# Performance work log

Hardware: AMD Instinct MI355X
Metric: run time of the kernel (lower is better)

## Reference

```python
import jax, jax.numpy as jnp
import numpy as np

N = 50000   # nodes
E = 600000  # edges
D = 128     # emb_dim
L = 5       # num_layers
ATOM_DIMS = np.array([119, 4, 11, 13, 11, 7, 13, 2, 9]) + 5   # per-feature vocab (+5 as in source)
BOND_DIMS = np.array([7, 22, 2]) + 5
BL_CENTERS = np.arange(0.0, 2.0, 0.1, dtype=np.float32)   # 20 centers, gamma 10
PR_CENTERS = np.arange(0.0, 1.0, 0.05, dtype=np.float32)  # 20 centers, gamma 1
BL_GAMMA = 10.0
PR_GAMMA = 1.0
BN_EPS = 1e-5


def setup_inputs() -> dict:
    key = jax.random.key(0)
    ks = jax.random.split(key, 16)
    scale = 1.0 / np.sqrt(D)
    atom_off = jnp.asarray(np.concatenate([[0], np.cumsum(ATOM_DIMS)[:-1]]), jnp.int32)
    bond_off = jnp.asarray(np.concatenate([[0], np.cumsum(BOND_DIMS)[:-1]]), jnp.int32)
    return {
        "x": jax.random.randint(ks[0], (N, 9), 0, 7, dtype=jnp.int32),
        "edge_index": jax.random.randint(ks[1], (2, E), 0, N, dtype=jnp.int32),
        "edge_attr_int": jax.random.randint(ks[2], (E, 3), 0, 7, dtype=jnp.int32),
        "edge_attr_float": jax.random.uniform(ks[3], (E, 2), dtype=jnp.float32),
        "atom_off": atom_off,
        "bond_off": bond_off,
        "atom_emb": jax.random.normal(ks[4], (int(ATOM_DIMS.sum()), D), jnp.float32) * scale,
        "bond_emb": jax.random.normal(ks[5], (L, int(BOND_DIMS.sum()), D), jnp.float32) * scale,
        "W_bl": jax.random.normal(ks[6], (L, len(BL_CENTERS), D), jnp.float32) * scale,
        "b_bl": jnp.zeros((L, D), jnp.float32),
        "W_pr": jax.random.normal(ks[7], (L, len(PR_CENTERS), D), jnp.float32) * scale,
        "b_pr": jnp.zeros((L, D), jnp.float32),
        "mlp_W1": jax.random.normal(ks[8], (L, D, D), jnp.float32) * scale,
        "mlp_b1": jnp.zeros((L, D), jnp.float32),
        "bn1_g": jnp.ones((L, D), jnp.float32),
        "bn1_b": jnp.zeros((L, D), jnp.float32),
        "mlp_W2": jax.random.normal(ks[9], (L, D, D), jnp.float32) * scale,
        "mlp_b2": jnp.zeros((L, D), jnp.float32),
        "eps_gin": jnp.zeros((L,), jnp.float32),
        "bn_g": jnp.ones((L, D), jnp.float32),
        "bn_b": jnp.zeros((L, D), jnp.float32),
    }


def _bn(h, g, b):
    # BatchNorm1d, training-mode batch statistics over the node axis
    m = h.mean(0)
    v = h.var(0)
    return (h - m) * jax.lax.rsqrt(v + BN_EPS) * g + b


def _rbf(x, centers, gamma):
    # exp(-gamma * (x - c)^2): [E] -> [E, n_centers]
    return jnp.exp(-gamma * jnp.square(x[:, None] - centers[None, :]))


def reference(x, edge_index, edge_attr_int, edge_attr_float, atom_off, bond_off,
              atom_emb, bond_emb, W_bl, b_bl, W_pr, b_pr,
              mlp_W1, mlp_b1, bn1_g, bn1_b, mlp_W2, mlp_b2,
              eps_gin, bn_g, bn_b):
    # AtomEncoder: sum of 9 categorical embeddings (flat table + offsets)
    h = atom_emb[x + atom_off[None, :]].sum(1)  # [N, D]
    src, dst = edge_index[0], edge_index[1]
    bl = _rbf(edge_attr_float[:, 0], jnp.asarray(BL_CENTERS), BL_GAMMA)  # [E, 20]
    pr = _rbf(edge_attr_float[:, 1], jnp.asarray(PR_CENTERS), PR_GAMMA)  # [E, 20]
    for l in range(L):
        # per-layer edge embedding: BondEncoder + BondFloatRBF
        e = bond_emb[l][edge_attr_int + bond_off[None, :]].sum(1)
        e = e + bl @ W_bl[l] + b_bl[l] + pr @ W_pr[l] + b_pr[l]
        # GINConv (aggr='add'): mlp((1+eps)*x + sum_j relu(x_j + e_ij))
        msg = jax.nn.relu(h[src] + e)                       # [E, D]
        agg = jax.ops.segment_sum(msg, dst, num_segments=N)  # [N, D]
        z = (1.0 + eps_gin[l]) * h + agg
        z = z @ mlp_W1[l] + mlp_b1[l]
        z = jax.nn.relu(_bn(z, bn1_g[l], bn1_b[l]))
        z = z @ mlp_W2[l] + mlp_b2[l]
        # outer per-layer BatchNorm; ReLU except last layer (drop_ratio=0)
        z = _bn(z, bn_g[l], bn_b[l])
        if l < L - 1:
            z = jax.nn.relu(z)
        h = z
    return h  # JK='last'
```

## Files before the change

### kernel.cpp

```cpp
#include <hip/hip_runtime.h>
#include <hip/hip_bf16.h>

#define GN 50000
#define GE 600000
#define DD 128
#define TQ 4096
#define NBOND 2268
#define TROWS (2*(TQ+1) + NBOND)
#define SCB 49
#define NBANK 16
#define SSET (NBANK*256)
#define NB 782
#define LDK 136

typedef __attribute__((ext_vector_type(8))) short short8;
typedef __attribute__((ext_vector_type(4))) unsigned short ushort4v;
typedef __attribute__((ext_vector_type(4))) float floatx4;

__device__ __forceinline__ unsigned short f2b(float f) {
    __hip_bfloat16 h = __float2bfloat16(f);
    return __builtin_bit_cast(unsigned short, h);
}
__device__ __forceinline__ float b2f_lo(unsigned int u) { return __uint_as_float(u << 16); }
__device__ __forceinline__ float b2f_hi(unsigned int u) { return __uint_as_float(u & 0xffff0000u); }
__device__ __forceinline__ float bs2f(short s) {
    return __uint_as_float(((unsigned int)(unsigned short)s) << 16);
}

__global__ __launch_bounds__(256) void atom_kernel(
    const int* __restrict__ x, const int* __restrict__ atom_off,
    const float* __restrict__ atom_emb, unsigned short* __restrict__ h)
{
    int t = blockIdx.x * 256 + threadIdx.x;
    if (t >= GN * DD) return;
    int n = t >> 7, d = t & 127;
    float s = 0.f;
#pragma unroll
    for (int f = 0; f < 9; f++) {
        int idx = x[n * 9 + f] + atom_off[f];
        s += atom_emb[idx * DD + d];
    }
    h[t] = f2b(s);
}

__global__ __launch_bounds__(256) void hist_kernel(const int* __restrict__ ei, int* __restrict__ count)
{
    int e = blockIdx.x * 256 + threadIdx.x;
    if (e < GE) atomicAdd(&count[ei[GE + e]], 1);
}

__global__ __launch_bounds__(1024) void scan1_kernel(
    const int* __restrict__ count, int* __restrict__ row_start, int* __restrict__ blocksum)
{
    __shared__ int sh[1024];
    int t = threadIdx.x;
    int idx = blockIdx.x * 1024 + t;
    int v = (idx < GN) ? count[idx] : 0;
    sh[t] = v;
    __syncthreads();
    for (int off = 1; off < 1024; off <<= 1) {
        int u = (t >= off) ? sh[t - off] : 0;
        __syncthreads();
        sh[t] += u;
        __syncthreads();
    }
    if (idx <= GN) row_start[idx] = (t == 0) ? 0 : sh[t - 1];
    if (t == 1023) blocksum[blockIdx.x] = sh[1023];
}

__global__ __launch_bounds__(64) void scan2_kernel(
    const int* __restrict__ blocksum, int* __restrict__ blockoff)
{
    int t = threadIdx.x;
    int v = (t < SCB) ? blocksum[t] : 0;
#pragma unroll
    for (int off = 1; off < 64; off <<= 1) {
        int u = __shfl_up(v, off);
        if (t >= off) v += u;
    }
    int e = __shfl_up(v, 1);
    if (t == 0) e = 0;
    if (t < SCB) blockoff[t] = e;
}

__global__ __launch_bounds__(1024) void scan3_kernel(
    int* __restrict__ row_start, const int* __restrict__ blockoff)
{
    int idx = blockIdx.x * 1024 + threadIdx.x;
    if (idx <= GN) row_start[idx] += blockoff[blockIdx.x];
}

__global__ __launch_bounds__(256) void scatter_kernel(
    const int* __restrict__ ei, const int* __restrict__ eai, const float* __restrict__ eaf,
    const int* __restrict__ row_start, int* __restrict__ fill, int4* __restrict__ ep)
{
    int e = blockIdx.x * 256 + threadIdx.x;
    if (e < GE) {
        int d = ei[GE + e];
        int p = row_start[d] + atomicAdd(&fill[d], 1);
        int src = ei[e];
        float x1 = eaf[2 * e], x2 = eaf[2 * e + 1];
        int q1 = (int)(x1 * (float)TQ + 0.5f); q1 = min(max(q1, 0), TQ);
        int q2 = (int)(x2 * (float)TQ + 0.5f); q2 = min(max(q2, 0), TQ);
        int b0 = eai[3 * e], b1 = eai[3 * e + 1], b2 = eai[3 * e + 2];
        ep[p] = make_int4(src, q1 | (q2 << 16), (b0 * 27 + b1) * 7 + b2, 0);
    }
}

__global__ __launch_bounds__(128) void tables_kernel(
    const float* __restrict__ W_bl, const float* __restrict__ b_bl,
    const float* __restrict__ W_pr, const float* __restrict__ b_pr,
    const float* __restrict__ bond_emb, const int* __restrict__ bond_off,
    unsigned short* __restrict__ tbl_bl, unsigned short* __restrict__ tbl_pr,
    unsigned short* __restrict__ tbl_bond)
{
    int l = blockIdx.x / TROWS;
    int b = blockIdx.x % TROWS;
    int d = threadIdx.x;
    const float* W_bl_l = W_bl + (size_t)l * 20 * DD;
    const float* W_pr_l = W_pr + (size_t)l * 20 * DD;
    const float* bemb_l = bond_emb + (size_t)l * 46 * DD;
    if (b < (TQ + 1)) {
        float xq = b * (1.0f / TQ);
        float s = b_bl[(size_t)l * DD + d] + b_pr[(size_t)l * DD + d];
#pragma unroll
        for (int k = 0; k < 20; k++) {
            float dl = xq - 0.1f * k;
            s += __expf(-10.f * dl * dl) * W_bl_l[k * DD + d];
        }
        tbl_bl[((size_t)l * (TQ + 1) + b) * DD + d] = f2b(s);
    } else if (b < 2 * (TQ + 1)) {
        int q = b - (TQ + 1);
        float xq = q * (1.0f / TQ);
        float s = 0.f;
#pragma unroll
        for (int k = 0; k < 20; k++) {
            float dl = xq - 0.05f * k;
            s += __expf(-dl * dl) * W_pr_l[k * DD + d];
        }
        tbl_pr[((size_t)l * (TQ + 1) + q) * DD + d] = f2b(s);
    } else {
        int r = b - 2 * (TQ + 1);
        int b0 = r / 189;
        int rem = r % 189;
        int b1 = rem / 7, b2 = rem % 7;
        tbl_bond[((size_t)l * NBOND + r) * DD + d] =
            f2b(bemb_l[(b0 + bond_off[0]) * DD + d]
              + bemb_l[(b1 + bond_off[1]) * DD + d]
              + bemb_l[(b2 + bond_off[2]) * DD + d]);
    }
}

__global__ __launch_bounds__(256) void wfrag_kernel(
    const float* __restrict__ W1, const float* __restrict__ W2,
    unsigned short* __restrict__ wf_hi, unsigned short* __restrict__ wf_lo)
{
    int t = blockIdx.x * 256 + threadIdx.x;
    if (t >= 10 * 2048) return;
    int mat = t >> 11;
    int rem = t & 2047;
    int kt = rem >> 9;
    int rem2 = rem & 511;
    int nt = rem2 >> 6;
    int lane = rem2 & 63;
    const float* src = (mat & 1) ? (W2 + (size_t)(mat >> 1) * DD * DD)
                                 : (W1 + (size_t)(mat >> 1) * DD * DD);
    int n = nt * 16 + (lane & 15);
    int k0 = kt * 32 + (lane >> 4) * 8;
    size_t base = (size_t)mat * 16384 + (size_t)((kt * 8 + nt) * 64 + lane) * 8;
#pragma unroll
    for (int j = 0; j < 8; j++) {
        float w = src[(size_t)(k0 + j) * DD + n];
        unsigned short hi = f2b(w);
        wf_hi[base + j] = hi;
        wf_lo[base + j] = f2b(w - bs2f((short)hi));
    }
}

template <int BN>
__global__ __launch_bounds__(256) void edge_kernel(
    const int4* __restrict__ ep,
    const unsigned short* __restrict__ tbl_bl, const unsigned short* __restrict__ tbl_pr,
    const unsigned short* __restrict__ tbl_bond,
    const unsigned short* __restrict__ hsrc, const int* __restrict__ row_start,
    const float* __restrict__ eps_gin, int layer,
    const float* __restrict__ stats_prev, const float* __restrict__ g_prev,
    const float* __restrict__ b_prev,
    float* __restrict__ A)
{
    __shared__ float sc_s[DD], tr_s[DD];
    int tid = threadIdx.x;
    if (BN) {
        if (tid < DD) {
            float s = 0.f, q = 0.f;
#pragma unroll
            for (int bk = 0; bk < NBANK; bk++) {
                s += stats_prev[bk * 256 + tid];
                q += stats_prev[bk * 256 + 128 + tid];
            }
            float m = s * (1.0f / GN);
            float v = q * (1.0f / GN) - m * m;
            float sc = g_prev[tid] * rsqrtf(v + 1e-5f);
            sc_s[tid] = sc;
            tr_s[tid] = b_prev[tid] - m * sc;
        }
        __syncthreads();
    }

    int wid = __builtin_amdgcn_readfirstlane(tid >> 6);
    int lane = tid & 63;
    float sc0 = 1.f, tr0 = 0.f, sc1 = 1.f, tr1 = 0.f;
    if (BN) {
        sc0 = sc_s[2 * lane];     tr0 = tr_s[2 * lane];
        sc1 = sc_s[2 * lane + 1]; tr1 = tr_s[2 * lane + 1];
    }

    int n = blockIdx.x * 4 + wid;
    int s0 = __builtin_amdgcn_readfirstlane(row_start[n]);
    int s1 = __builtin_amdgcn_readfirstlane(row_start[n + 1]);
    const unsigned int* hu = (const unsigned int*)hsrc;
    const unsigned int* tb = (const unsigned int*)tbl_bl;
    const unsigned int* tp = (const unsigned int*)tbl_pr;
    const unsigned int* tg = (const unsigned int*)tbl_bond;
    float a0 = 0.f, a1 = 0.f;

    auto meta = [&](int pb, int4 (&mm)[4]) {
#pragma unroll
        for (int j = 0; j < 4; j++) mm[j] = ep[pb + j];
    };
    auto issue = [&](const int4 (&mm)[4], unsigned int (&ub)[4], unsigned int (&up)[4],
                     unsigned int (&ug)[4], unsigned int (&uh)[4]) {
#pragma unroll
        for (int j = 0; j < 4; j++) {
            ub[j] = tb[(size_t)(mm[j].y & 0xffff) * 64 + lane];
            up[j] = tp[(size_t)((unsigned)mm[j].y >> 16) * 64 + lane];
            ug[j] = tg[(size_t)mm[j].z * 64 + lane];
            uh[j] = hu[(size_t)mm[j].x * 64 + lane];
        }
    };
    auto consume = [&](const unsigned int (&ub)[4], const unsigned int (&up)[4],
                       const unsigned int (&ug)[4], const unsigned int (&uh)[4]) {
#pragma unroll
        for (int j = 0; j < 4; j++) {
            float h0, h1;
            if (BN) {
                h0 = fmaxf(fmaf(b2f_lo(uh[j]), sc0, tr0), 0.f);
                h1 = fmaxf(fmaf(b2f_hi(uh[j]), sc1, tr1), 0.f);
            } else {
                h0 = b2f_lo(uh[j]);
                h1 = b2f_hi(uh[j]);
            }
            a0 += fmaxf(h0 + b2f_lo(ub[j]) + b2f_lo(up[j]) + b2f_lo(ug[j]), 0.f);
            a1 += fmaxf(h1 + b2f_hi(ub[j]) + b2f_hi(up[j]) + b2f_hi(ug[j]), 0.f);
        }
    };

    int cnt = s1 - s0;
    int nfull = cnt >> 2;
    {
        int4 mA[4], mB[4];
        unsigned int ubA[4], upA[4], ugA[4], uhA[4];
        unsigned int ubB[4], upB[4], ugB[4], uhB[4];
        if (nfull > 0) {
            meta(s0, mA);
            issue(mA, ubA, upA, ugA, uhA);
            int i = 1;
            for (; i + 1 < nfull; i += 2) {
                meta(s0 + i * 4, mB);
                meta(s0 + (i + 1) * 4, mA);
                issue(mB, ubB, upB, ugB, uhB);
                consume(ubA, upA, ugA, uhA);
                issue(mA, ubA, upA, ugA, uhA);
                consume(ubB, upB, ugB, uhB);
            }
            if (i < nfull) {
                meta(s0 + i * 4, mB);
                issue(mB, ubB, upB, ugB, uhB);
                consume(ubA, upA, ugA, uhA);
                consume(ubB, upB, ugB, uhB);
            } else {
                consume(ubA, upA, ugA, uhA);
            }
        }
    }
    for (int p = s0 + nfull * 4; p < s1; p++) {
        int4 m0 = ep[p];
        unsigned int ub0 = tb[(size_t)(m0.y & 0xffff) * 64 + lane];
        unsigned int up0 = tp[(size_t)((unsigned)m0.y >> 16) * 64 + lane];
        unsigned int ug0 = tg[(size_t)m0.z * 64 + lane];
        unsigned int uh0 = hu[(size_t)m0.x * 64 + lane];
        float h00, h01;
        if (BN) {
            h00 = fmaxf(fmaf(b2f_lo(uh0), sc0, tr0), 0.f);
            h01 = fmaxf(fmaf(b2f_hi(uh0), sc1, tr1), 0.f);
        } else {
            h00 = b2f_lo(uh0);
            h01 = b2f_hi(uh0);
        }
        a0 += fmaxf(h00 + b2f_lo(ub0) + b2f_lo(up0) + b2f_lo(ug0), 0.f);
        a1 += fmaxf(h01 + b2f_hi(ub0) + b2f_hi(up0) + b2f_hi(ug0), 0.f);
    }

    float eps1 = 1.f + eps_gin[layer];
    unsigned int un = hu[(size_t)n * 64 + lane];
    float n0, n1;
    if (BN) {
        n0 = fmaxf(fmaf(b2f_lo(un), sc0, tr0), 0.f);
        n1 = fmaxf(fmaf(b2f_hi(un), sc1, tr1), 0.f);
    } else {
        n0 = b2f_lo(un);
        n1 = b2f_hi(un);
    }
    a0 += eps1 * n0;
    a1 += eps1 * n1;
    float2 o; o.x = a0; o.y = a1;
    *(float2*)(A + (size_t)n * DD + 2 * lane) = o;
}

template <int MODE>
__global__ __launch_bounds__(256) void gemm_kernel(
    const float* __restrict__ Asrc,
    const unsigned short* __restrict__ wf_hi, const unsigned short* __restrict__ wf_lo,
    const float* __restrict__ bias,
    unsigned short* __restrict__ Cbf, float* __restrict__ Cf32, int out_bf16,
    const float* __restrict__ stats_in, const float* __restrict__ bn_g,
    const float* __restrict__ bn_b, float* __restrict__ stats_out)
{
    __shared__ unsigned short Ahi[64 * LDK];
    __shared__ unsigned short Alo[64 * LDK];
    __shared__ float sc_s[DD], tr_s[DD];
    int tid = threadIdx.x, wid = tid >> 6, lane = tid & 63;
    int row0 = blockIdx.x * 64;

    if (MODE == 1) {
        if (tid < DD) {
            float s = 0.f, q = 0.f;
#pragma unroll
            for (int bk = 0; bk < NBANK; bk++) {
                s += stats_in[bk * 256 + tid];
                q += stats_in[bk * 256 + 128 + tid];
            }
            float m = s * (1.0f / GN);
            float v = q * (1.0f / GN) - m * m;
            float sc = bn_g[tid] * rsqrtf(v + 1e-5f);
            sc_s[tid] = sc;
            tr_s[tid] = bn_b[tid] - m * sc;
        }
        __syncthreads();
    }

    {
        const float* g = Asrc + (size_t)row0 * DD;
#pragma unroll
        for (int i = 0; i < 8; i++) {
            int idx = i * 1024 + tid * 4;
            float4 v = *(const float4*)(g + idx);
            int r = idx >> 7, c = idx & 127;
            if (MODE == 1) {
                v.x = fmaxf(v.x * sc_s[c]     + tr_s[c],     0.f);
                v.y = fmaxf(v.y * sc_s[c + 1] + tr_s[c + 1], 0.f);
                v.z = fmaxf(v.z * sc_s[c + 2] + tr_s[c + 2], 0.f);
                v.w = fmaxf(v.w * sc_s[c + 3] + tr_s[c + 3], 0.f);
            }
            ushort4v hi, lo;
            hi[0] = f2b(v.x); lo[0] = f2b(v.x - bs2f((short)hi[0]));
            hi[1] = f2b(v.y); lo[1] = f2b(v.y - bs2f((short)hi[1]));
            hi[2] = f2b(v.z); lo[2] = f2b(v.z - bs2f((short)hi[2]));
            hi[3] = f2b(v.w); lo[3] = f2b(v.w - bs2f((short)hi[3]));
            *(ushort4v*)(Ahi + r * LDK + c) = hi;
            *(ushort4v*)(Alo + r * LDK + c) = lo;
        }
    }
    __syncthreads();

    int quad = lane >> 4, l16 = lane & 15;
    floatx4 acc[4][2];
#pragma unroll
    for (int rt = 0; rt < 4; rt++)
#pragma unroll
        for (int nt = 0; nt < 2; nt++) acc[rt][nt] = (floatx4){0.f, 0.f, 0.f, 0.f};

    const short8* bhp = (const short8*)wf_hi;
    const short8* blp = (const short8*)wf_lo;
#pragma unroll
    for (int kt = 0; kt < 4; kt++) {
        short8 ahi[4], alo[4];
        int kb = kt * 32 + quad * 8;
#pragma unroll
        for (int rt = 0; rt < 4; rt++) {
            int ro = (rt * 16 + l16) * LDK + kb;
            ahi[rt] = *(const short8*)(Ahi + ro);
            alo[rt] = *(const short8*)(Alo + ro);
        }
#pragma unroll
        for (int nt = 0; nt < 2; nt++) {
            int ntg = wid * 2 + nt;
            short8 bhi = bhp[(kt * 8 + ntg) * 64 + lane];
            short8 blo = blp[(kt * 8 + ntg) * 64 + lane];
#pragma unroll
            for (int rt = 0; rt < 4; rt++) {
                acc[rt][nt] = __builtin_amdgcn_mfma_f32_16x16x32_bf16(ahi[rt], bhi, acc[rt][nt], 0, 0, 0);
                acc[rt][nt] = __builtin_amdgcn_mfma_f32_16x16x32_bf16(alo[rt], bhi, acc[rt][nt], 0, 0, 0);
                acc[rt][nt] = __builtin_amdgcn_mfma_f32_16x16x32_bf16(ahi[rt], blo, acc[rt][nt], 0, 0, 0);
            }
        }
    }

    int bank = blockIdx.x & (NBANK - 1);
#pragma unroll
    for (int nt = 0; nt < 2; nt++) {
        int col = (wid * 2 + nt) * 16 + l16;
        float bv = bias[col];
        float s = 0.f, q = 0.f;
#pragma unroll
        for (int rt = 0; rt < 4; rt++) {
#pragma unroll
            for (int v = 0; v < 4; v++) {
                int r = row0 + rt * 16 + quad * 4 + v;
                float o = acc[rt][nt][v] + bv;
                if (r < GN) {
                    s += o; q += o * o;
                    if (MODE == 1 && out_bf16) Cbf[(size_t)r * DD + col] = f2b(o);
                    else                       Cf32[(size_t)r * DD + col] = o;
                }
            }
        }
        s += __shfl_xor(s, 16); s += __shfl_xor(s, 32);
        q += __shfl_xor(q, 16); q += __shfl_xor(q, 32);
        if (lane < 16) {
            atomicAdd(&stats_out[bank * 256 + col], s);
            atomicAdd(&stats_out[bank * 256 + 128 + col], q);
        }
    }
}

__global__ __launch_bounds__(256) void bn_apply_kernel(
    const float* __restrict__ Z, const float* __restrict__ stats2,
    const float* __restrict__ g, const float* __restrict__ b,
    float* __restrict__ fout)
{
    __shared__ float sc_s[DD], tr_s[DD];
    int tid = threadIdx.x;
    if (tid < DD) {
        float s = 0.f, q = 0.f;
#pragma unroll
        for (int bk = 0; bk < NBANK; bk++) {
            s += stats2[bk * 256 + tid];
            q += stats2[bk * 256 + 128 + tid];
        }
        float m = s * (1.0f / GN);
        float v = q * (1.0f / GN) - m * m;
        float sc = g[tid] * rsqrtf(v + 1e-5f);
        sc_s[tid] = sc;
        tr_s[tid] = b[tid] - m * sc;
    }
    __syncthreads();
    const int total = GN * DD;
    for (int t = blockIdx.x * 256 + tid; t < total; t += gridDim.x * 256) {
        int c = t & 127;
        fout[t] = Z[t] * sc_s[c] + tr_s[c];
    }
}

extern "C" void kernel_launch(void* const* d_in, const int* in_sizes, int n_in,
                              void* d_out, int out_size, void* d_ws, size_t ws_size,
                              hipStream_t stream)
{
    const int*   x        = (const int*)d_in[0];
    const int*   ei       = (const int*)d_in[1];
    const int*   eai      = (const int*)d_in[2];
    const float* eaf      = (const float*)d_in[3];
    const int*   atom_off = (const int*)d_in[4];
    const int*   bond_off = (const int*)d_in[5];
    const float* atom_emb = (const float*)d_in[6];
    const float* bond_emb = (const float*)d_in[7];
    const float* W_bl     = (const float*)d_in[8];
    const float* b_bl     = (const float*)d_in[9];
    const float* W_pr     = (const float*)d_in[10];
    const float* b_pr     = (const float*)d_in[11];
    const float* W1       = (const float*)d_in[12];
    const float* b1       = (const float*)d_in[13];
    const float* bn1g     = (const float*)d_in[14];
    const float* bn1b     = (const float*)d_in[15];
    const float* W2       = (const float*)d_in[16];
    const float* b2       = (const float*)d_in[17];
    const float* eps_gin  = (const float*)d_in[18];
    const float* bng      = (const float*)d_in[19];
    const float* bnb      = (const float*)d_in[20];
    float* out = (float*)d_out;

    char* p = (char*)d_ws;
    unsigned short* h_bf  = (unsigned short*)p;  p += (size_t)GN * DD * 2;
    unsigned short* z2_bf = (unsigned short*)p;  p += (size_t)GN * DD * 2;
    float* A              = (float*)p;           p += (size_t)GN * DD * 4;
    float* z1             = (float*)p;           p += (size_t)GN * DD * 4;
    float* z2f            = (float*)p;           p += (size_t)GN * DD * 4;
    unsigned short* tbl_bl   = (unsigned short*)p;  p += (size_t)5 * (TQ + 1) * DD * 2;
    unsigned short* tbl_pr   = (unsigned short*)p;  p += (size_t)5 * (TQ + 1) * DD * 2;
    unsigned short* tbl_bond = (unsigned short*)p;  p += (size_t)5 * NBOND * DD * 2;
    unsigned short* wf_hi    = (unsigned short*)p;  p += (size_t)10 * 16384 * 2;
    unsigned short* wf_lo    = (unsigned short*)p;  p += (size_t)10 * 16384 * 2;
    float* stats_all = (float*)p;  p += (size_t)10 * SSET * 4;
    int* count    = (int*)p;    p += (size_t)GN * 4;
    int* fill     = (int*)p;    p += (size_t)GN * 4;
    int* row_start= (int*)p;    p += (size_t)(GN + 1) * 4;
    int* blocksum = (int*)p;    p += (size_t)SCB * 4;
    int* blockoff = (int*)p;    p += (size_t)SCB * 4;
    p = (char*)(((size_t)p + 15) & ~(size_t)15);
    int4* ep      = (int4*)p;   p += (size_t)GE * 16;

    hipMemsetAsync(count, 0, (size_t)GN * 4, stream);
    hipMemsetAsync(fill,  0, (size_t)GN * 4, stream);
    hipMemsetAsync(stats_all, 0, (size_t)10 * SSET * 4, stream);

    hist_kernel<<<(GE + 255) / 256, 256, 0, stream>>>(ei, count);
    scan1_kernel<<<SCB, 1024, 0, stream>>>(count, row_start, blocksum);
    scan2_kernel<<<1, 64, 0, stream>>>(blocksum, blockoff);
    scan3_kernel<<<SCB, 1024, 0, stream>>>(row_start, blockoff);
    scatter_kernel<<<(GE + 255) / 256, 256, 0, stream>>>(ei, eai, eaf, row_start, fill, ep);
    atom_kernel<<<(GN * DD + 255) / 256, 256, 0, stream>>>(x, atom_off, atom_emb, h_bf);
    wfrag_kernel<<<80, 256, 0, stream>>>(W1, W2, wf_hi, wf_lo);
    tables_kernel<<<5 * TROWS, 128, 0, stream>>>(
        W_bl, b_bl, W_pr, b_pr, bond_emb, bond_off, tbl_bl, tbl_pr, tbl_bond);

    for (int l = 0; l < 5; l++) {
        float* stats1 = stats_all + (size_t)(2 * l + 0) * SSET;
        float* stats2 = stats_all + (size_t)(2 * l + 1) * SSET;
        float* stats2_prev = stats_all + (size_t)(2 * (l - 1) + 1) * SSET;

        if (l == 0) {
            edge_kernel<0><<<GN / 4, 256, 0, stream>>>(
                ep, tbl_bl, tbl_pr, tbl_bond,
                h_bf, row_start, eps_gin, l,
                stats_all, bng, bnb, A);
        } else {
            edge_kernel<1><<<GN / 4, 256, 0, stream>>>(
                ep,
                tbl_bl + (size_t)l * (TQ + 1) * DD,
                tbl_pr + (size_t)l * (TQ + 1) * DD,
                tbl_bond + (size_t)l * NBOND * DD,
                z2_bf, row_start, eps_gin, l,
                stats2_prev,
                bng + (size_t)(l - 1) * DD,
                bnb + (size_t)(l - 1) * DD,
                A);
        }

        gemm_kernel<0><<<NB, 256, 0, stream>>>(
            A, wf_hi + (size_t)(l * 2 + 0) * 16384, wf_lo + (size_t)(l * 2 + 0) * 16384,
            b1 + (size_t)l * DD, nullptr, z1, 0,
            nullptr, nullptr, nullptr, stats1);

        gemm_kernel<1><<<NB, 256, 0, stream>>>(
            z1, wf_hi + (size_t)(l * 2 + 1) * 16384, wf_lo + (size_t)(l * 2 + 1) * 16384,
            b2 + (size_t)l * DD, z2_bf, z2f, (l < 4) ? 1 : 0,
            stats1, bn1g + (size_t)l * DD, bn1b + (size_t)l * DD, stats2);
    }

    bn_apply_kernel<<<1024, 256, 0, stream>>>(
        z2f, stats_all + (size_t)9 * SSET, bng + (size_t)4 * DD, bnb + (size_t)4 * DD, out);
}
```

Baseline: 668.7 us.

## Fuse edge aggregation and both MLP GEMMs into one cooperative per-layer kernel

Each layer's edge gather-aggregate, first GEMM with BN statistics, BN1+ReLU and second GEMM now run in a single cooperative kernel. Grid-wide syncs separate the phases, and the first GEMM's output stays in registers and LDS instead of a global z1 buffer. The last layer also applies the final BatchNorm in-kernel, which drops the separate bn_apply launch. This removes per-layer launches and the z1 global round trip, but the edge phase now runs as a grid-stride loop over only 782 blocks, so fewer waves are available to hide gather latency. The fallback path keeps the old kernels, with a simplified, unpipelined edge loop.

```diff
diff --git a/kernel.cpp b/kernel.cpp
--- a/kernel.cpp
+++ b/kernel.cpp
@@ -1,5 +1,8 @@
 #include <hip/hip_runtime.h>
 #include <hip/hip_bf16.h>
+#include <hip/hip_cooperative_groups.h>
+
+namespace cg = cooperative_groups;
 
 #define GN 50000
 #define GE 600000
@@ -177,6 +180,364 @@
     }
 }
 
+template <int L0, int LAST>
+__global__ __launch_bounds__(256, 4) void layer_kernel(
+    const int4* __restrict__ ep,
+    const unsigned short* __restrict__ tbl_bl, const unsigned short* __restrict__ tbl_pr,
+    const unsigned short* __restrict__ tbl_bond,
+    const unsigned short* __restrict__ hsrc, const int* __restrict__ row_start,
+    const float* __restrict__ eps_gin, int layer,
+    const float* __restrict__ stats_prev, const float* __restrict__ g_prev,
+    const float* __restrict__ b_prev,
+    float* __restrict__ A,
+    const unsigned short* __restrict__ wf1_hi, const unsigned short* __restrict__ wf1_lo,
+    const unsigned short* __restrict__ wf2_hi, const unsigned short* __restrict__ wf2_lo,
+    const float* __restrict__ bias1, const float* __restrict__ bias2,
+    float* __restrict__ stats1, float* __restrict__ stats2,
+    const float* __restrict__ bn1_g, const float* __restrict__ bn1_b,
+    const float* __restrict__ bn2_g, const float* __restrict__ bn2_b,
+    unsigned short* __restrict__ z2bf, float* __restrict__ out)
+{
+    __shared__ unsigned short Ahi[64 * LDK];
+    __shared__ unsigned short Alo[64 * LDK];
+    __shared__ float sc_s[DD], tr_s[DD];
+    cg::grid_group grid = cg::this_grid();
+    int tid = threadIdx.x, wid = tid >> 6, lane = tid & 63;
+
+    if (!L0) {
+        if (tid < DD) {
+            float s = 0.f, q = 0.f;
+#pragma unroll
+            for (int bk = 0; bk < NBANK; bk++) {
+                s += stats_prev[bk * 256 + tid];
+                q += stats_prev[bk * 256 + 128 + tid];
+            }
+            float m = s * (1.0f / GN);
+            float v = q * (1.0f / GN) - m * m;
+            float sc = g_prev[tid] * rsqrtf(v + 1e-5f);
+            sc_s[tid] = sc;
+            tr_s[tid] = b_prev[tid] - m * sc;
+        }
+        __syncthreads();
+    }
+    float sc0 = 1.f, tr0 = 0.f, sc1 = 1.f, tr1 = 0.f;
+    if (!L0) {
+        sc0 = sc_s[2 * lane];     tr0 = tr_s[2 * lane];
+        sc1 = sc_s[2 * lane + 1]; tr1 = tr_s[2 * lane + 1];
+    }
+
+    {
+        const unsigned int* hu = (const unsigned int*)hsrc;
+        const unsigned int* tb = (const unsigned int*)tbl_bl;
+        const unsigned int* tp = (const unsigned int*)tbl_pr;
+        const unsigned int* tg = (const unsigned int*)tbl_bond;
+        float eps1 = 1.f + eps_gin[layer];
+        int gw = blockIdx.x * 4 + wid;
+
+        for (int n = gw; n < GN; n += NB * 4) {
+            int s0 = __builtin_amdgcn_readfirstlane(row_start[n]);
+            int s1 = __builtin_amdgcn_readfirstlane(row_start[n + 1]);
+            float a0 = 0.f, a1 = 0.f;
+
+            auto meta = [&](int pb, int4 (&mm)[4]) {
+#pragma unroll
+                for (int j = 0; j < 4; j++) mm[j] = ep[pb + j];
+            };
+            auto issue = [&](const int4 (&mm)[4], unsigned int (&ub)[4], unsigned int (&up)[4],
+                             unsigned int (&ug)[4], unsigned int (&uh)[4]) {
+#pragma unroll
+                for (int j = 0; j < 4; j++) {
+                    ub[j] = tb[(size_t)(mm[j].y & 0xffff) * 64 + lane];
+                    up[j] = tp[(size_t)((unsigned)mm[j].y >> 16) * 64 + lane];
+                    ug[j] = tg[(size_t)mm[j].z * 64 + lane];
+                    uh[j] = hu[(size_t)mm[j].x * 64 + lane];
+                }
+            };
+            auto consume = [&](const unsigned int (&ub)[4], const unsigned int (&up)[4],
+                               const unsigned int (&ug)[4], const unsigned int (&uh)[4]) {
+#pragma unroll
+                for (int j = 0; j < 4; j++) {
+                    float h0, h1;
+                    if (!L0) {
+                        h0 = fmaxf(fmaf(b2f_lo(uh[j]), sc0, tr0), 0.f);
+                        h1 = fmaxf(fmaf(b2f_hi(uh[j]), sc1, tr1), 0.f);
+                    } else {
+                        h0 = b2f_lo(uh[j]);
+                        h1 = b2f_hi(uh[j]);
+                    }
+                    a0 += fmaxf(h0 + b2f_lo(ub[j]) + b2f_lo(up[j]) + b2f_lo(ug[j]), 0.f);
+                    a1 += fmaxf(h1 + b2f_hi(ub[j]) + b2f_hi(up[j]) + b2f_hi(ug[j]), 0.f);
+                }
+            };
+
+            int nfull = (s1 - s0) >> 2;
+            {
+                int4 mA[4], mB[4];
+                unsigned int ubA[4], upA[4], ugA[4], uhA[4];
+                unsigned int ubB[4], upB[4], ugB[4], uhB[4];
+                if (nfull > 0) {
+                    meta(s0, mA);
+                    issue(mA, ubA, upA, ugA, uhA);
+                    int i = 1;
+                    for (; i + 1 < nfull; i += 2) {
+                        meta(s0 + i * 4, mB);
+                        meta(s0 + (i + 1) * 4, mA);
+                        issue(mB, ubB, upB, ugB, uhB);
+                        consume(ubA, upA, ugA, uhA);
+                        issue(mA, ubA, upA, ugA, uhA);
+                        consume(ubB, upB, ugB, uhB);
+                    }
+                    if (i < nfull) {
+                        meta(s0 + i * 4, mB);
+                        issue(mB, ubB, upB, ugB, uhB);
+                        consume(ubA, upA, ugA, uhA);
+                        consume(ubB, upB, ugB, uhB);
+                    } else {
+                        consume(ubA, upA, ugA, uhA);
+                    }
+                }
+            }
+            for (int p = s0 + nfull * 4; p < s1; p++) {
+                int4 m0 = ep[p];
+                unsigned int ub0 = tb[(size_t)(m0.y & 0xffff) * 64 + lane];
+                unsigned int up0 = tp[(size_t)((unsigned)m0.y >> 16) * 64 + lane];
+                unsigned int ug0 = tg[(size_t)m0.z * 64 + lane];
+                unsigned int uh0 = hu[(size_t)m0.x * 64 + lane];
+                float h00, h01;
+                if (!L0) {
+                    h00 = fmaxf(fmaf(b2f_lo(uh0), sc0, tr0), 0.f);
+                    h01 = fmaxf(fmaf(b2f_hi(uh0), sc1, tr1), 0.f);
+                } else {
+                    h00 = b2f_lo(uh0);
+                    h01 = b2f_hi(uh0);
+                }
+                a0 += fmaxf(h00 + b2f_lo(ub0) + b2f_lo(up0) + b2f_lo(ug0), 0.f);
+                a1 += fmaxf(h01 + b2f_hi(ub0) + b2f_hi(up0) + b2f_hi(ug0), 0.f);
+            }
+
+            unsigned int un = hu[(size_t)n * 64 + lane];
+            float n0, n1;
+            if (!L0) {
+                n0 = fmaxf(fmaf(b2f_lo(un), sc0, tr0), 0.f);
+                n1 = fmaxf(fmaf(b2f_hi(un), sc1, tr1), 0.f);
+            } else {
+                n0 = b2f_lo(un);
+                n1 = b2f_hi(un);
+            }
+            a0 += eps1 * n0;
+            a1 += eps1 * n1;
+            float2 o; o.x = a0; o.y = a1;
+            *(float2*)(A + (size_t)n * DD + 2 * lane) = o;
+        }
+    }
+    __threadfence();
+    grid.sync();
+
+    int row0 = blockIdx.x * 64;
+    {
+        const float* g = A + (size_t)row0 * DD;
+#pragma unroll
+        for (int i = 0; i < 8; i++) {
+            int idx = i * 1024 + tid * 4;
+            float4 v = *(const float4*)(g + idx);
+            int r = idx >> 7, c = idx & 127;
+            ushort4v hi, lo;
+            hi[0] = f2b(v.x); lo[0] = f2b(v.x - bs2f((short)hi[0]));
+            hi[1] = f2b(v.y); lo[1] = f2b(v.y - bs2f((short)hi[1]));
+            hi[2] = f2b(v.z); lo[2] = f2b(v.z - bs2f((short)hi[2]));
+            hi[3] = f2b(v.w); lo[3] = f2b(v.w - bs2f((short)hi[3]));
+            *(ushort4v*)(Ahi + r * LDK + c) = hi;
+            *(ushort4v*)(Alo + r * LDK + c) = lo;
+        }
+    }
+    __syncthreads();
+
+    int quad = lane >> 4, l16 = lane & 15;
+    int bank = blockIdx.x & (NBANK - 1);
+    floatx4 acc1[4][2];
+#pragma unroll
+    for (int rt = 0; rt < 4; rt++)
+#pragma unroll
+        for (int nt = 0; nt < 2; nt++) acc1[rt][nt] = (floatx4){0.f, 0.f, 0.f, 0.f};
+    {
+        const short8* bhp = (const short8*)wf1_hi;
+        const short8* blp = (const short8*)wf1_lo;
+#pragma unroll
+        for (int kt = 0; kt < 4; kt++) {
+            short8 ahi[4], alo[4];
+            int kb = kt * 32 + quad * 8;
+#pragma unroll
+            for (int rt = 0; rt < 4; rt++) {
+                int ro = (rt * 16 + l16) * LDK + kb;
+                ahi[rt] = *(const short8*)(Ahi + ro);
+                alo[rt] = *(const short8*)(Alo + ro);
+            }
+#pragma unroll
+            for (int nt = 0; nt < 2; nt++) {
+                int ntg = wid * 2 + nt;
+                short8 bhi = bhp[(kt * 8 + ntg) * 64 + lane];
+                short8 blo = blp[(kt * 8 + ntg) * 64 + lane];
+#pragma unroll
+                for (int rt = 0; rt < 4; rt++) {
+                    acc1[rt][nt] = __builtin_amdgcn_mfma_f32_16x16x32_bf16(ahi[rt], bhi, acc1[rt][nt], 0, 0, 0);
+                    acc1[rt][nt] = __builtin_amdgcn_mfma_f32_16x16x32_bf16(alo[rt], bhi, acc1[rt][nt], 0, 0, 0);
+                    acc1[rt][nt] = __builtin_amdgcn_mfma_f32_16x16x32_bf16(ahi[rt], blo, acc1[rt][nt], 0, 0, 0);
+                }
+            }
+        }
+    }
+#pragma unroll
+    for (int nt = 0; nt < 2; nt++) {
+        int col = (wid * 2 + nt) * 16 + l16;
+        float bv = bias1[col];
+        float s = 0.f, q = 0.f;
+#pragma unroll
+        for (int rt = 0; rt < 4; rt++) {
+#pragma unroll
+            for (int v = 0; v < 4; v++) {
+                int r = row0 + rt * 16 + quad * 4 + v;
+                float o = acc1[rt][nt][v] + bv;
+                if (r < GN) { s += o; q += o * o; }
+            }
+        }
+        s += __shfl_xor(s, 16); s += __shfl_xor(s, 32);
+        q += __shfl_xor(q, 16); q += __shfl_xor(q, 32);
+        if (lane < 16) {
+            atomicAdd(&stats1[bank * 256 + col], s);
+            atomicAdd(&stats1[bank * 256 + 128 + col], q);
+        }
+    }
+    __threadfence();
+    grid.sync();
+
+    if (tid < DD) {
+        float s = 0.f, q = 0.f;
+#pragma unroll
+        for (int bk = 0; bk < NBANK; bk++) {
+            s += stats1[bk * 256 + tid];
+            q += stats1[bk * 256 + 128 + tid];
+        }
+        float m = s * (1.0f / GN);
+        float v = q * (1.0f / GN) - m * m;
+        float sc = bn1_g[tid] * rsqrtf(v + 1e-5f);
+        sc_s[tid] = sc;
+        tr_s[tid] = bn1_b[tid] - m * sc;
+    }
+    __syncthreads();
+#pragma unroll
+    for (int nt = 0; nt < 2; nt++) {
+        int col = (wid * 2 + nt) * 16 + l16;
+        float bv = bias1[col];
+        float sc = sc_s[col], tr = tr_s[col];
+#pragma unroll
+        for (int rt = 0; rt < 4; rt++) {
+#pragma unroll
+            for (int v = 0; v < 4; v++) {
+                int lr = rt * 16 + quad * 4 + v;
+                float o = acc1[rt][nt][v] + bv;
+                float h = fmaxf(o * sc + tr, 0.f);
+                unsigned short hi = f2b(h);
+                Ahi[lr * LDK + col] = hi;
+                Alo[lr * LDK + col] = f2b(h - bs2f((short)hi));
+            }
+        }
+    }
+    __syncthreads();
+
+    floatx4 acc2[4][2];
+#pragma unroll
+    for (int rt = 0; rt < 4; rt++)
+#pragma unroll
+        for (int nt = 0; nt < 2; nt++) acc2[rt][nt] = (floatx4){0.f, 0.f, 0.f, 0.f};
+    {
+        const short8* bhp = (const short8*)wf2_hi;
+        const short8* blp = (const short8*)wf2_lo;
+#pragma unroll
+        for (int kt = 0; kt < 4; kt++) {
+            short8 ahi[4], alo[4];
+            int kb = kt * 32 + quad * 8;
+#pragma unroll
+            for (int rt = 0; rt < 4; rt++) {
+                int ro = (rt * 16 + l16) * LDK + kb;
+                ahi[rt] = *(const short8*)(Ahi + ro);
+                alo[rt] = *(const short8*)(Alo + ro);
+            }
+#pragma unroll
+            for (int nt = 0; nt < 2; nt++) {
+                int ntg = wid * 2 + nt;
+                short8 bhi = bhp[(kt * 8 + ntg) * 64 + lane];
+                short8 blo = blp[(kt * 8 + ntg) * 64 + lane];
+#pragma unroll
+                for (int rt = 0; rt < 4; rt++) {
+                    acc2[rt][nt] = __builtin_amdgcn_mfma_f32_16x16x32_bf16(ahi[rt], bhi, acc2[rt][nt], 0, 0, 0);
+                    acc2[rt][nt] = __builtin_amdgcn_mfma_f32_16x16x32_bf16(alo[rt], bhi, acc2[rt][nt], 0, 0, 0);
+                    acc2[rt][nt] = __builtin_amdgcn_mfma_f32_16x16x32_bf16(ahi[rt], blo, acc2[rt][nt], 0, 0, 0);
+                }
+            }
+        }
+    }
+#pragma unroll
+    for (int nt = 0; nt < 2; nt++) {
+        int col = (wid * 2 + nt) * 16 + l16;
+        float bv = bias2[col];
+        float s = 0.f, q = 0.f;
+#pragma unroll
+        for (int rt = 0; rt < 4; rt++) {
+#pragma unroll
+            for (int v = 0; v < 4; v++) {
+                int r = row0 + rt * 16 + quad * 4 + v;
+                float o = acc2[rt][nt][v] + bv;
+                if (r < GN) {
+                    s += o; q += o * o;
+                    if (!LAST) z2bf[(size_t)r * DD + col] = f2b(o);
+                }
+            }
+        }
+        s += __shfl_xor(s, 16); s += __shfl_xor(s, 32);
+        q += __shfl_xor(q, 16); q += __shfl_xor(q, 32);
+        if (lane < 16) {
+            atomicAdd(&stats2[bank * 256 + col], s);
+            atomicAdd(&stats2[bank * 256 + 128 + col], q);
+        }
+    }
+
+    if (LAST) {
+        __threadfence();
+        grid.sync();
+        if (tid < DD) {
+            float s = 0.f, q = 0.f;
+#pragma unroll
+            for (int bk = 0; bk < NBANK; bk++) {
+                s += stats2[bk * 256 + tid];
+                q += stats2[bk * 256 + 128 + tid];
+            }
+            float m = s * (1.0f / GN);
+            float v = q * (1.0f / GN) - m * m;
+            float sc = bn2_g[tid] * rsqrtf(v + 1e-5f);
+            sc_s[tid] = sc;
+            tr_s[tid] = bn2_b[tid] - m * sc;
+        }
+        __syncthreads();
+#pragma unroll
+        for (int nt = 0; nt < 2; nt++) {
+            int col = (wid * 2 + nt) * 16 + l16;
+            float bv = bias2[col];
+            float sc = sc_s[col], tr = tr_s[col];
+#pragma unroll
+            for (int rt = 0; rt < 4; rt++) {
+#pragma unroll
+                for (int v = 0; v < 4; v++) {
+                    int r = row0 + rt * 16 + quad * 4 + v;
+                    if (r < GN) {
+                        float o = acc2[rt][nt][v] + bv;
+                        out[(size_t)r * DD + col] = o * sc + tr;
+                    }
+                }
+            }
+        }
+    }
+}
+
 template <int BN>
 __global__ __launch_bounds__(256) void edge_kernel(
     const int4* __restrict__ ep,
@@ -206,7 +567,6 @@
         }
         __syncthreads();
     }
-
     int wid = __builtin_amdgcn_readfirstlane(tid >> 6);
     int lane = tid & 63;
     float sc0 = 1.f, tr0 = 0.f, sc1 = 1.f, tr1 = 0.f;
@@ -214,7 +574,6 @@
         sc0 = sc_s[2 * lane];     tr0 = tr_s[2 * lane];
         sc1 = sc_s[2 * lane + 1]; tr1 = tr_s[2 * lane + 1];
     }
-
     int n = blockIdx.x * 4 + wid;
     int s0 = __builtin_amdgcn_readfirstlane(row_start[n]);
     int s1 = __builtin_amdgcn_readfirstlane(row_start[n + 1]);
@@ -223,67 +582,7 @@
     const unsigned int* tp = (const unsigned int*)tbl_pr;
     const unsigned int* tg = (const unsigned int*)tbl_bond;
     float a0 = 0.f, a1 = 0.f;
-
-    auto meta = [&](int pb, int4 (&mm)[4]) {
-#pragma unroll
-        for (int j = 0; j < 4; j++) mm[j] = ep[pb + j];
-    };
-    auto issue = [&](const int4 (&mm)[4], unsigned int (&ub)[4], unsigned int (&up)[4],
-                     unsigned int (&ug)[4], unsigned int (&uh)[4]) {
-#pragma unroll
-        for (int j = 0; j < 4; j++) {
-            ub[j] = tb[(size_t)(mm[j].y & 0xffff) * 64 + lane];
-            up[j] = tp[(size_t)((unsigned)mm[j].y >> 16) * 64 + lane];
-            ug[j] = tg[(size_t)mm[j].z * 64 + lane];
-            uh[j] = hu[(size_t)mm[j].x * 64 + lane];
-        }
-    };
-    auto consume = [&](const unsigned int (&ub)[4], const unsigned int (&up)[4],
-                       const unsigned int (&ug)[4], const unsigned int (&uh)[4]) {
-#pragma unroll
-        for (int j = 0; j < 4; j++) {
-            float h0, h1;
-            if (BN) {
-                h0 = fmaxf(fmaf(b2f_lo(uh[j]), sc0, tr0), 0.f);
-                h1 = fmaxf(fmaf(b2f_hi(uh[j]), sc1, tr1), 0.f);
-            } else {
-                h0 = b2f_lo(uh[j]);
-                h1 = b2f_hi(uh[j]);
-            }
-            a0 += fmaxf(h0 + b2f_lo(ub[j]) + b2f_lo(up[j]) + b2f_lo(ug[j]), 0.f);
-            a1 += fmaxf(h1 + b2f_hi(ub[j]) + b2f_hi(up[j]) + b2f_hi(ug[j]), 0.f);
-        }
-    };
-
-    int cnt = s1 - s0;
-    int nfull = cnt >> 2;
-    {
-        int4 mA[4], mB[4];
-        unsigned int ubA[4], upA[4], ugA[4], uhA[4];
-        unsigned int ubB[4], upB[4], ugB[4], uhB[4];
-        if (nfull > 0) {
-            meta(s0, mA);
-            issue(mA, ubA, upA, ugA, uhA);
-            int i = 1;
-            for (; i + 1 < nfull; i += 2) {
-                meta(s0 + i * 4, mB);
-                meta(s0 + (i + 1) * 4, mA);
-                issue(mB, ubB, upB, ugB, uhB);
-                consume(ubA, upA, ugA, uhA);
-                issue(mA, ubA, upA, ugA, uhA);
-                consume(ubB, upB, ugB, uhB);
-            }
-            if (i < nfull) {
-                meta(s0 + i * 4, mB);
-                issue(mB, ubB, upB, ugB, uhB);
-                consume(ubA, upA, ugA, uhA);
-                consume(ubB, upB, ugB, uhB);
-            } else {
-                consume(ubA, upA, ugA, uhA);
-            }
-        }
-    }
-    for (int p = s0 + nfull * 4; p < s1; p++) {
+    for (int p = s0; p < s1; p++) {
         int4 m0 = ep[p];
         unsigned int ub0 = tb[(size_t)(m0.y & 0xffff) * 64 + lane];
         unsigned int up0 = tp[(size_t)((unsigned)m0.y >> 16) * 64 + lane];
@@ -300,7 +599,6 @@
         a0 += fmaxf(h00 + b2f_lo(ub0) + b2f_lo(up0) + b2f_lo(ug0), 0.f);
         a1 += fmaxf(h01 + b2f_hi(ub0) + b2f_hi(up0) + b2f_hi(ug0), 0.f);
     }
-
     float eps1 = 1.f + eps_gin[layer];
     unsigned int un = hu[(size_t)n * 64 + lane];
     float n0, n1;
@@ -331,7 +629,6 @@
     __shared__ float sc_s[DD], tr_s[DD];
     int tid = threadIdx.x, wid = tid >> 6, lane = tid & 63;
     int row0 = blockIdx.x * 64;
-
     if (MODE == 1) {
         if (tid < DD) {
             float s = 0.f, q = 0.f;
@@ -348,7 +645,6 @@
         }
         __syncthreads();
     }
-
     {
         const float* g = Asrc + (size_t)row0 * DD;
 #pragma unroll
@@ -372,14 +668,12 @@
         }
     }
     __syncthreads();
-
     int quad = lane >> 4, l16 = lane & 15;
     floatx4 acc[4][2];
 #pragma unroll
     for (int rt = 0; rt < 4; rt++)
 #pragma unroll
         for (int nt = 0; nt < 2; nt++) acc[rt][nt] = (floatx4){0.f, 0.f, 0.f, 0.f};
-
     const short8* bhp = (const short8*)wf_hi;
     const short8* blp = (const short8*)wf_lo;
 #pragma unroll
@@ -405,7 +699,6 @@
             }
         }
     }
-
     int bank = blockIdx.x & (NBANK - 1);
 #pragma unroll
     for (int nt = 0; nt < 2; nt++) {
@@ -523,40 +816,91 @@
     tables_kernel<<<5 * TROWS, 128, 0, stream>>>(
         W_bl, b_bl, W_pr, b_pr, bond_emb, bond_off, tbl_bl, tbl_pr, tbl_bond);
 
+    bool legacy = false;
     for (int l = 0; l < 5; l++) {
         float* stats1 = stats_all + (size_t)(2 * l + 0) * SSET;
         float* stats2 = stats_all + (size_t)(2 * l + 1) * SSET;
         float* stats2_prev = stats_all + (size_t)(2 * (l - 1) + 1) * SSET;
 
-        if (l == 0) {
-            edge_kernel<0><<<GN / 4, 256, 0, stream>>>(
-                ep, tbl_bl, tbl_pr, tbl_bond,
-                h_bf, row_start, eps_gin, l,
-                stats_all, bng, bnb, A);
-        } else {
-            edge_kernel<1><<<GN / 4, 256, 0, stream>>>(
-                ep,
-                tbl_bl + (size_t)l * (TQ + 1) * DD,
-                tbl_pr + (size_t)l * (TQ + 1) * DD,
-                tbl_bond + (size_t)l * NBOND * DD,
-                z2_bf, row_start, eps_gin, l,
-                stats2_prev,
-                bng + (size_t)(l - 1) * DD,
-                bnb + (size_t)(l - 1) * DD,
-                A);
-        }
-
-        gemm_kernel<0><<<NB, 256, 0, stream>>>(
-            A, wf_hi + (size_t)(l * 2 + 0) * 16384, wf_lo + (size_t)(l * 2 + 0) * 16384,
-            b1 + (size_t)l * DD, nullptr, z1, 0,
-            nullptr, nullptr, nullptr, stats1);
-
-        gemm_kernel<1><<<NB, 256, 0, stream>>>(
-            z1, wf_hi + (size_t)(l * 2 + 1) * 16384, wf_lo + (size_t)(l * 2 + 1) * 16384,
-            b2 + (size_t)l * DD, z2_bf, z2f, (l < 4) ? 1 : 0,
-            stats1, bn1g + (size_t)l * DD, bn1b + (size_t)l * DD, stats2);
-    }
-
-    bn_apply_kernel<<<1024, 256, 0, stream>>>(
-        z2f, stats_all + (size_t)9 * SSET, bng + (size_t)4 * DD, bnb + (size_t)4 * DD, out);
-}
+        if (!legacy) {
+            const int4* ep_a = ep;
+            const unsigned short* tbl_bl_a = tbl_bl + (size_t)l * (TQ + 1) * DD;
+            const unsigned short* tbl_pr_a = tbl_pr + (size_t)l * (TQ + 1) * DD;
+            const unsigned short* tbl_bond_a = tbl_bond + (size_t)l * NBOND * DD;
+            const unsigned short* hsrc_a = (l == 0) ? h_bf : z2_bf;
+            const int* rs_a = row_start;
+            const float* eps_a = eps_gin;
+            int layer_a = l;
+            const float* sp_a = (l > 0) ? stats2_prev : stats_all;
+            const float* gp_a = bng + (size_t)(l > 0 ? l - 1 : 0) * DD;
+            const float* bp_a = bnb + (size_t)(l > 0 ? l - 1 : 0) * DD;
+            float* A_a = A;
+            const unsigned short* w1h_a = wf_hi + (size_t)(l * 2 + 0) * 16384;
+            const unsigned short* w1l_a = wf_lo + (size_t)(l * 2 + 0) * 16384;
+            const unsigned short* w2h_a = wf_hi + (size_t)(l * 2 + 1) * 16384;
+            const unsigned short* w2l_a = wf_lo + (size_t)(l * 2 + 1) * 16384;
+            const float* b1_a = b1 + (size_t)l * DD;
+            const float* b2_a = b2 + (size_t)l * DD;
+            float* s1_a = stats1;
+            float* s2_a = stats2;
+            const float* bn1g_a = bn1g + (size_t)l * DD;
+            const float* bn1b_a = bn1b + (size_t)l * DD;
+            const float* bn2g_a = bng + (size_t)l * DD;
+            const float* bn2b_a = bnb + (size_t)l * DD;
+            unsigned short* z2_a = z2_bf;
+            float* out_a = out;
+            void* args[] = {
+                (void*)&ep_a, (void*)&tbl_bl_a, (void*)&tbl_pr_a, (void*)&tbl_bond_a,
+                (void*)&hsrc_a, (void*)&rs_a, (void*)&eps_a, (void*)&layer_a,
+                (void*)&sp_a, (void*)&gp_a, (void*)&bp_a, (void*)&A_a,
+                (void*)&w1h_a, (void*)&w1l_a, (void*)&w2h_a, (void*)&w2l_a,
+                (void*)&b1_a, (void*)&b2_a, (void*)&s1_a, (void*)&s2_a,
+                (void*)&bn1g_a, (void*)&bn1b_a, (void*)&bn2g_a, (void*)&bn2b_a,
+                (void*)&z2_a, (void*)&out_a };
+            hipError_t e;
+            if (l == 0)
+                e = hipLaunchCooperativeKernel((const void*)&layer_kernel<1, 0>,
+                                               dim3(NB), dim3(256), args, 0, stream);
+            else if (l < 4)
+                e = hipLaunchCooperativeKernel((const void*)&layer_kernel<0, 0>,
+                                               dim3(NB), dim3(256), args, 0, stream);
+            else
+                e = hipLaunchCooperativeKernel((const void*)&layer_kernel<0, 1>,
+                                               dim3(NB), dim3(256), args, 0, stream);
+            if (e != hipSuccess) legacy = true;
+        }
+
+        if (legacy) {
+            if (l == 0) {
+                edge_kernel<0><<<GN / 4, 256, 0, stream>>>(
+                    ep, tbl_bl, tbl_pr, tbl_bond,
+                    h_bf, row_start, eps_gin, l,
+                    stats_all, bng, bnb, A);
+            } else {
+                edge_kernel<1><<<GN / 4, 256, 0, stream>>>(
+                    ep,
+                    tbl_bl + (size_t)l * (TQ + 1) * DD,
+                    tbl_pr + (size_t)l * (TQ + 1) * DD,
+                    tbl_bond + (size_t)l * NBOND * DD,
+                    z2_bf, row_start, eps_gin, l,
+                    stats2_prev,
+                    bng + (size_t)(l - 1) * DD,
+                    bnb + (size_t)(l - 1) * DD,
+                    A);
+            }
+            gemm_kernel<0><<<NB, 256, 0, stream>>>(
+                A, wf_hi + (size_t)(l * 2 + 0) * 16384, wf_lo + (size_t)(l * 2 + 0) * 16384,
+                b1 + (size_t)l * DD, nullptr, z1, 0,
+                nullptr, nullptr, nullptr, stats1);
+            gemm_kernel<1><<<NB, 256, 0, stream>>>(
+                z1, wf_hi + (size_t)(l * 2 + 1) * 16384, wf_lo + (size_t)(l * 2 + 1) * 16384,
+                b2 + (size_t)l * DD, z2_bf, z2f, (l < 4) ? 1 : 0,
+                stats1, bn1g + (size_t)l * DD, bn1b + (size_t)l * DD, stats2);
+        }
+    }
+
+    if (legacy) {
+        bn_apply_kernel<<<1024, 256, 0, stream>>>(
+            z2f, stats_all + (size_t)9 * SSET, bng + (size_t)4 * DD, bnb + (size_t)4 * DD, out);
+    }
+}
```

After: 2.414 ms. +261.0%, slower.
